# Kernel optimization log

Hardware: AMD Instinct MI355X
Metric: run time of the kernel (lower is better)

Reference implementation:

```python
import jax, jax.numpy as jnp
import numpy as np

STATE_DIM = 256
LATENT_DIM = 64
HIDDEN = 64
NUM_EMB = 2048
BATCH = 32768


def setup_inputs() -> dict:
    key = jax.random.key(0)
    ks = jax.random.split(key, 10)
    s = lambda *sh: 1.0 / np.sqrt(sh[0])
    return {
        "x": jax.random.normal(ks[0], (BATCH, STATE_DIM), dtype=jnp.float32),
        # encoder: Linear(state_dim, 64) -> ReLU -> Linear(64, latent_dim)
        "enc_w1": jax.random.uniform(ks[1], (STATE_DIM, HIDDEN), jnp.float32, -s(STATE_DIM), s(STATE_DIM)),
        "enc_b1": jax.random.uniform(ks[2], (HIDDEN,), jnp.float32, -s(STATE_DIM), s(STATE_DIM)),
        "enc_w2": jax.random.uniform(ks[3], (HIDDEN, LATENT_DIM), jnp.float32, -s(HIDDEN), s(HIDDEN)),
        "enc_b2": jax.random.uniform(ks[4], (LATENT_DIM,), jnp.float32, -s(HIDDEN), s(HIDDEN)),
        # codebook
        "emb": jax.random.normal(ks[5], (NUM_EMB, LATENT_DIM), dtype=jnp.float32),
        # decoder: Linear(latent_dim, 64) -> ReLU -> Linear(64, state_dim)
        "dec_w1": jax.random.uniform(ks[6], (LATENT_DIM, HIDDEN), jnp.float32, -s(LATENT_DIM), s(LATENT_DIM)),
        "dec_b1": jax.random.uniform(ks[7], (HIDDEN,), jnp.float32, -s(LATENT_DIM), s(LATENT_DIM)),
        "dec_w2": jax.random.uniform(ks[8], (HIDDEN, STATE_DIM), jnp.float32, -s(HIDDEN), s(HIDDEN)),
        "dec_b2": jax.random.uniform(ks[9], (STATE_DIM,), jnp.float32, -s(HIDDEN), s(HIDDEN)),
    }


def reference(x, enc_w1, enc_b1, enc_w2, enc_b2, emb, dec_w1, dec_b1, dec_w2, dec_b2):
    # encoder MLP: z_e [B, latent]
    h = jax.nn.relu(x @ enc_w1 + enc_b1)
    z_e = h @ enc_w2 + enc_b2
    # squared euclidean distances to codebook, expanded form: [B, K]
    # ||z - e||^2 = ||z||^2 - 2 z.e + ||e||^2  (same argmin as broadcast form)
    d = (jnp.sum(z_e * z_e, axis=1, keepdims=True)
         - 2.0 * (z_e @ emb.T)
         + jnp.sum(emb * emb, axis=1)[None, :])
    z_q_idx = jnp.argmin(d, axis=1)           # [B]
    z_q = emb[z_q_idx]                        # [B, latent]
    # decoder MLP
    hd = jax.nn.relu(z_q @ dec_w1 + dec_b1)
    x_recon = hd @ dec_w2 + dec_b2
    return (x_recon, z_e, z_q)
```

## Files before the change

### kernel.cpp

```cpp
#include <hip/hip_runtime.h>

#define BATCH   32768
#define SD      256
#define LD      64
#define HDIM    64
#define NEMB    2048
#define REFINE_THR_Q 5e-4f

typedef short  short8 __attribute__((ext_vector_type(8)));
typedef float  f32x4  __attribute__((ext_vector_type(4)));

__device__ __forceinline__ unsigned short f2bf(float f) {
    unsigned int u = __float_as_uint(f);
    u = (u + 0x7FFFu + ((u >> 16) & 1u)) >> 16;
    return (unsigned short)u;
}
__device__ __forceinline__ float bf2f(unsigned short h) {
    return __uint_as_float(((unsigned int)h) << 16);
}

__global__ __launch_bounds__(256) void k0_all(const float* __restrict__ emb,
                                              const float* __restrict__ dw1,
                                              const float* __restrict__ dw2,
                                              const float* __restrict__ ew1,
                                              const float* __restrict__ ew2,
                                              float* __restrict__ e2q,
                                              unsigned short* __restrict__ eh,
                                              unsigned short* __restrict__ el,
                                              unsigned short* __restrict__ w1h,
                                              unsigned short* __restrict__ w1l,
                                              unsigned short* __restrict__ w2h,
                                              unsigned short* __restrict__ w2l,
                                              unsigned short* __restrict__ w1eh,
                                              unsigned short* __restrict__ w1em,
                                              unsigned short* __restrict__ w1el,
                                              unsigned short* __restrict__ w2eh,
                                              unsigned short* __restrict__ w2em,
                                              unsigned short* __restrict__ w2el) {
    int b = blockIdx.x;
    int t = threadIdx.x;
    if (b < 8) {
        int k = b * 256 + t;
        const float* er = emb + (size_t)k * LD;
        unsigned short hrow[LD], lrow[LD];
        float s = 0.f;
#pragma unroll
        for (int q = 0; q < LD; ++q) {
            float v = er[q];
            s += v * v;
            unsigned short h = f2bf(v);
            hrow[q] = h;
            lrow[q] = f2bf(v - bf2f(h));
        }
        e2q[k] = -0.5f * s;
        short8* dh = (short8*)(eh + (size_t)k * LD);
        short8* dl = (short8*)(el + (size_t)k * LD);
#pragma unroll
        for (int q = 0; q < 8; ++q) {
            dh[q] = *(short8*)&hrow[q * 8];
            dl[q] = *(short8*)&lrow[q * 8];
        }
    } else if (b < 24) {
        int e = (b - 8) * 256 + t;
        int j = e >> 6, k = e & 63;
        float v = dw1[k * HDIM + j];
        unsigned short h = f2bf(v);
        w1h[e] = h; w1l[e] = f2bf(v - bf2f(h));
    } else if (b < 88) {
        int e = (b - 24) * 256 + t;
        int j = e >> 6, k = e & 63;
        float v = dw2[k * SD + j];
        unsigned short h = f2bf(v);
        w2h[e] = h; w2l[e] = f2bf(v - bf2f(h));
    } else if (b < 152) {
        int e = (b - 88) * 256 + t;
        int j = e >> 8, k = e & 255;
        float v = ew1[k * HDIM + j];
        unsigned short h = f2bf(v);
        float r1 = v - bf2f(h);
        unsigned short m = f2bf(r1);
        float r2 = r1 - bf2f(m);
        w1eh[e] = h; w1em[e] = m; w1el[e] = f2bf(r2);
    } else {
        int e = (b - 152) * 256 + t;
        int j = e >> 6, k = e & 63;
        float v = ew2[k * LD + j];
        unsigned short h = f2bf(v);
        float r1 = v - bf2f(h);
        unsigned short m = f2bf(r1);
        float r2 = r1 - bf2f(m);
        w2eh[e] = h; w2em[e] = m; w2el[e] = f2bf(r2);
    }
}

#define MF(Afr, Bfr, C) __builtin_amdgcn_mfma_f32_16x16x32_bf16(Afr, Bfr, C, 0, 0, 0)

__global__ __launch_bounds__(256, 2) void k_enc(const float* __restrict__ x,
                                                const unsigned short* __restrict__ w1eh,
                                                const unsigned short* __restrict__ w1em,
                                                const unsigned short* __restrict__ w1el,
                                                const float* __restrict__ b1,
                                                const unsigned short* __restrict__ w2eh,
                                                const unsigned short* __restrict__ w2em,
                                                const unsigned short* __restrict__ w2el,
                                                const float* __restrict__ b2,
                                                float* __restrict__ zOut,
                                                unsigned short* __restrict__ zh,
                                                unsigned short* __restrict__ zl) {
    __shared__ float hds[4][16 * 68];
    int tid  = threadIdx.x;
    int lane = tid & 63;
    int w    = tid >> 6;
    int lo   = lane & 15;
    int hi   = lane >> 4;
    int rb   = blockIdx.x * 64 + w * 16;
    int row  = rb + lo;

    f32x4 c1[4];
#pragma unroll
    for (int jt = 0; jt < 4; ++jt) {
        float bj = b1[jt * 16 + lo];
        f32x4 c = {bj, bj, bj, bj};
        c1[jt] = c;
    }

#pragma unroll
    for (int kt = 0; kt < 8; ++kt) {
        const float* xp = x + (size_t)row * SD + kt * 32 + hi * 8;
        float4 a4 = *(const float4*)xp;
        float4 b4 = *(const float4*)(xp + 4);
        float v[8] = {a4.x, a4.y, a4.z, a4.w, b4.x, b4.y, b4.z, b4.w};
        unsigned short sh[8], sm[8], sl[8];
#pragma unroll
        for (int q = 0; q < 8; ++q) {
            unsigned short h = f2bf(v[q]);
            float r1 = v[q] - bf2f(h);
            unsigned short m = f2bf(r1);
            float r2 = r1 - bf2f(m);
            sh[q] = h; sm[q] = m; sl[q] = f2bf(r2);
        }
        short8 ah = *(short8*)sh, am = *(short8*)sm, al = *(short8*)sl;
#pragma unroll
        for (int jt = 0; jt < 4; ++jt) {
            size_t wo = (size_t)(jt * 16 + lo) * SD + kt * 32 + hi * 8;
            short8 bh8 = *(const short8*)(w1eh + wo);
            short8 bm8 = *(const short8*)(w1em + wo);
            short8 bl8 = *(const short8*)(w1el + wo);
            f32x4 c = c1[jt];
            c = MF(al, bh8, c);
            c = MF(am, bm8, c);
            c = MF(ah, bl8, c);
            c = MF(am, bh8, c);
            c = MF(ah, bm8, c);
            c = MF(ah, bh8, c);
            c1[jt] = c;
        }
    }
#pragma unroll
    for (int jt = 0; jt < 4; ++jt)
#pragma unroll
        for (int r = 0; r < 4; ++r)
            hds[w][(hi * 4 + r) * 68 + jt * 16 + lo] = fmaxf(c1[jt][r], 0.f);
    __syncthreads();

    f32x4 c2[4];
#pragma unroll
    for (int jt = 0; jt < 4; ++jt) {
        float bj = b2[jt * 16 + lo];
        f32x4 c = {bj, bj, bj, bj};
        c2[jt] = c;
    }
#pragma unroll
    for (int kt = 0; kt < 2; ++kt) {
        float4 a4 = *(const float4*)&hds[w][lo * 68 + kt * 32 + hi * 8];
        float4 b4 = *(const float4*)&hds[w][lo * 68 + kt * 32 + hi * 8 + 4];
        float v[8] = {a4.x, a4.y, a4.z, a4.w, b4.x, b4.y, b4.z, b4.w};
        unsigned short sh[8], sm[8], sl[8];
#pragma unroll
        for (int q = 0; q < 8; ++q) {
            unsigned short h = f2bf(v[q]);
            float r1 = v[q] - bf2f(h);
            unsigned short m = f2bf(r1);
            float r2 = r1 - bf2f(m);
            sh[q] = h; sm[q] = m; sl[q] = f2bf(r2);
        }
        short8 ah = *(short8*)sh, am = *(short8*)sm, al = *(short8*)sl;
#pragma unroll
        for (int jt = 0; jt < 4; ++jt) {
            size_t wo = (size_t)(jt * 16 + lo) * LD + kt * 32 + hi * 8;
            short8 bh8 = *(const short8*)(w2eh + wo);
            short8 bm8 = *(const short8*)(w2em + wo);
            short8 bl8 = *(const short8*)(w2el + wo);
            f32x4 c = c2[jt];
            c = MF(al, bh8, c);
            c = MF(am, bm8, c);
            c = MF(ah, bl8, c);
            c = MF(am, bh8, c);
            c = MF(ah, bm8, c);
            c = MF(ah, bh8, c);
            c2[jt] = c;
        }
    }
#pragma unroll
    for (int jt = 0; jt < 4; ++jt) {
#pragma unroll
        for (int r = 0; r < 4; ++r) {
            float z = c2[jt][r];
            size_t o = (size_t)(rb + hi * 4 + r) * LD + jt * 16 + lo;
            zOut[o] = z;
            unsigned short hb = f2bf(z);
            zh[o] = hb;
            zl[o] = f2bf(z - bf2f(hb));
        }
    }
}

#define K2_LOAD(P, t) do {                                                  \
    const unsigned short* ph_ = ehp + (size_t)(t) * 16 * LD;                \
    const unsigned short* pl_ = elp + (size_t)(t) * 16 * LD;                \
    P##a0 = *(const short8*)(ph_);                                          \
    P##a1 = *(const short8*)(ph_ + 32);                                     \
    P##a2 = *(const short8*)(pl_);                                          \
    P##a3 = *(const short8*)(pl_ + 32);                                     \
    P##e2 = *(const f32x4*)(e2q + cbase + (t) * 16 + hi * 4);               \
} while (0)

#define K2_COMP(P, t) do {                                                  \
    f32x4 acc_[4];                                                          \
    _Pragma("unroll")                                                       \
    for (int g = 0; g < 4; ++g) {                                           \
        f32x4 c_;                                                           \
        c_ = __builtin_amdgcn_mfma_f32_16x16x32_bf16(P##a0, bh[g][0], P##e2, 0, 0, 0); \
        c_ = __builtin_amdgcn_mfma_f32_16x16x32_bf16(P##a1, bh[g][1], c_, 0, 0, 0);    \
        c_ = __builtin_amdgcn_mfma_f32_16x16x32_bf16(P##a2, bh[g][0], c_, 0, 0, 0);    \
        c_ = __builtin_amdgcn_mfma_f32_16x16x32_bf16(P##a3, bh[g][1], c_, 0, 0, 0);    \
        c_ = __builtin_amdgcn_mfma_f32_16x16x32_bf16(P##a0, bl[g][0], c_, 0, 0, 0);    \
        c_ = __builtin_amdgcn_mfma_f32_16x16x32_bf16(P##a1, bl[g][1], c_, 0, 0, 0);    \
        acc_[g] = c_;                                                       \
    }                                                                       \
    _Pragma("unroll")                                                       \
    for (int g = 0; g < 4; ++g) {                                           \
        float m_ = fmaxf(fmaxf(acc_[g][0], acc_[g][1]),                     \
                         fmaxf(acc_[g][2], acc_[g][3]));                    \
        bool win_ = (m_ > bb[g]);                                           \
        qv[g] = win_ ? acc_[g] : qv[g];                                     \
        tt[g] = win_ ? (t) : tt[g];                                         \
        b2v[g] = fmaxf(b2v[g], fminf(bb[g], m_));                           \
        bb[g] = fmaxf(bb[g], m_);                                           \
    }                                                                       \
} while (0)

__global__ __launch_bounds__(256, 2) void k2_mfma(const unsigned short* __restrict__ zh,
                                                  const unsigned short* __restrict__ zl,
                                                  const unsigned short* __restrict__ eh,
                                                  const unsigned short* __restrict__ el,
                                                  const float* __restrict__ e2q,
                                                  const float* __restrict__ zE,
                                                  const float* __restrict__ emb,
                                                  int* __restrict__ idx) {
    int tid  = threadIdx.x;
    int lane = tid & 63;
    int w    = tid >> 6;
    int rb   = blockIdx.x * 64;
    int lo   = lane & 15;
    int hi   = lane >> 4;

    short8 bh[4][2], bl[4][2];
#pragma unroll
    for (int g = 0; g < 4; ++g) {
        size_t zo = (size_t)(rb + g * 16 + lo) * LD + hi * 8;
        bh[g][0] = *(const short8*)(zh + zo);
        bh[g][1] = *(const short8*)(zh + zo + 32);
        bl[g][0] = *(const short8*)(zl + zo);
        bl[g][1] = *(const short8*)(zl + zo + 32);
    }

    float bb[4], b2v[4];
    f32x4 qv[4];
    int   tt[4];
#pragma unroll
    for (int g = 0; g < 4; ++g) {
        bb[g] = -3.0e38f; b2v[g] = -3.0e38f; tt[g] = 0;
        qv[g][0] = qv[g][1] = qv[g][2] = qv[g][3] = -3.0e38f;
    }

    const int cbase = w * (NEMB / 4);
    const unsigned short* ehp = eh + (size_t)(cbase + lo) * LD + hi * 8;
    const unsigned short* elp = el + (size_t)(cbase + lo) * LD + hi * 8;

    short8 Aa0, Aa1, Aa2, Aa3; f32x4 Ae2;
    short8 Ba0, Ba1, Ba2, Ba3; f32x4 Be2;
    short8 Ca0, Ca1, Ca2, Ca3; f32x4 Ce2;

    K2_LOAD(A, 0);
    K2_LOAD(B, 1);
    K2_LOAD(C, 2);

    for (int tb = 0; tb < 27; tb += 3) {
        K2_COMP(A, tb);     K2_LOAD(A, tb + 3);
        K2_COMP(B, tb + 1); K2_LOAD(B, tb + 4);
        K2_COMP(C, tb + 2); K2_LOAD(C, tb + 5);
    }
    K2_COMP(A, 27); K2_LOAD(A, 30);
    K2_COMP(B, 28); K2_LOAD(B, 31);
    K2_COMP(C, 29);
    K2_COMP(A, 30);
    K2_COMP(B, 31);

    float ss[4];
    int   ii[4];
#pragma unroll
    for (int g = 0; g < 4; ++g) {
        float s0 = qv[g][0], s1 = qv[g][1], s2 = qv[g][2], s3 = qv[g][3];
        float M01 = fmaxf(s0, s1), L01 = fminf(s0, s1);
        float M23 = fmaxf(s2, s3), L23 = fminf(s2, s3);
        int   d01 = (s1 > s0) ? 1 : 0;
        int   d23 = (s3 > s2) ? 3 : 2;
        bool  cp  = (M23 > M01);
        float within2 = fmaxf(fminf(M01, M23), cp ? L23 : L01);
        int   dd  = cp ? d23 : d01;
        ii[g] = cbase + tt[g] * 16 + hi * 4 + dd;
        ss[g] = fmaxf(b2v[g], within2);
    }

#pragma unroll
    for (int off = 16; off <= 32; off <<= 1) {
#pragma unroll
        for (int g = 0; g < 4; ++g) {
            float ob = __shfl_xor(bb[g], off);
            float os = __shfl_xor(ss[g], off);
            int   oi = __shfl_xor(ii[g], off);
            ss[g] = fmaxf(fmaxf(fminf(bb[g], ob), os), ss[g]);
            ii[g] = (ob > bb[g]) ? oi : ii[g];
            bb[g] = fmaxf(bb[g], ob);
        }
    }

    __shared__ float Lb[4][64];
    __shared__ float Ls[4][64];
    __shared__ int   Li[4][64];
    __shared__ int   flags[64];
    if (lane < 16) {
#pragma unroll
        for (int g = 0; g < 4; ++g) {
            Lb[w][g * 16 + lane] = bb[g];
            Ls[w][g * 16 + lane] = ss[g];
            Li[w][g * 16 + lane] = ii[g];
        }
    }
    __syncthreads();

    if (tid < 64) {
        float B = Lb[0][tid], S = Ls[0][tid];
        int   I = Li[0][tid];
#pragma unroll
        for (int w2 = 1; w2 < 4; ++w2) {
            float ob = Lb[w2][tid], os = Ls[w2][tid];
            int   oi = Li[w2][tid];
            S = fmaxf(fmaxf(fminf(B, ob), os), S);
            I = (ob > B) ? oi : I;
            B = fmaxf(B, ob);
        }
        idx[rb + tid] = I;
        flags[tid] = (B - S < REFINE_THR_Q) ? 1 : 0;
    }
    __syncthreads();

    __shared__ double sv[256];
    __shared__ int    sx[256];
    for (int r = 0; r < 64; ++r) {
        if (flags[r] == 0) continue;
        int rrow = rb + r;
        const float4* zr4 = (const float4*)(zE + (size_t)rrow * LD);
        float4 zv[16];
#pragma unroll
        for (int q = 0; q < 16; ++q) zv[q] = zr4[q];
        double best = 1.0e300;
        int bi = NEMB;
#pragma unroll 2
        for (int c = 0; c < 8; ++c) {
            int k = tid * 8 + c;
            const float4* er = (const float4*)(emb + (size_t)k * LD);
            double d0 = 0.0, d1 = 0.0, d2 = 0.0, d3 = 0.0;
#pragma unroll
            for (int q = 0; q < 16; ++q) {
                float4 e4 = er[q];
                double tx = (double)zv[q].x - (double)e4.x;
                double ty = (double)zv[q].y - (double)e4.y;
                double tz = (double)zv[q].z - (double)e4.z;
                double tw = (double)zv[q].w - (double)e4.w;
                d0 += tx * tx; d1 += ty * ty; d2 += tz * tz; d3 += tw * tw;
            }
            double d = (d0 + d1) + (d2 + d3);
            if (d < best) { best = d; bi = k; }
        }
        sv[tid] = best; sx[tid] = bi;
        __syncthreads();
        for (int s = 128; s > 0; s >>= 1) {
            if (tid < s) {
                if (sv[tid + s] < sv[tid] ||
                    (sv[tid + s] == sv[tid] && sx[tid + s] < sx[tid])) {
                    sv[tid] = sv[tid + s]; sx[tid] = sx[tid + s];
                }
            }
            __syncthreads();
        }
        if (tid == 0) idx[rrow] = sx[0];
        __syncthreads();
    }
}

__global__ __launch_bounds__(256, 2) void k_dec(const int* __restrict__ idx,
                                                const float* __restrict__ emb,
                                                const unsigned short* __restrict__ w1h,
                                                const unsigned short* __restrict__ w1l,
                                                const float* __restrict__ b1,
                                                const unsigned short* __restrict__ w2h,
                                                const unsigned short* __restrict__ w2l,
                                                const float* __restrict__ b2,
                                                float* __restrict__ xrec,
                                                float* __restrict__ zq) {
    __shared__ float hds[4][16 * 68];
    int tid  = threadIdx.x;
    int lane = tid & 63;
    int w    = tid >> 6;
    int lo   = lane & 15;
    int hi   = lane >> 4;
    int rb   = blockIdx.x * 64 + w * 16;
    int row  = rb + lo;
    int ix   = idx[row];

    short8 zah[2], zal[2];
    {
        const float* er  = emb + (size_t)ix * LD + hi * 8;
        float* zqr = zq + (size_t)row * LD + hi * 8;
#pragma unroll
        for (int kt = 0; kt < 2; ++kt) {
            float4 a = *(const float4*)(er + kt * 32);
            float4 b = *(const float4*)(er + kt * 32 + 4);
            *(float4*)(zqr + kt * 32) = a;
            *(float4*)(zqr + kt * 32 + 4) = b;
            float v[8] = {a.x, a.y, a.z, a.w, b.x, b.y, b.z, b.w};
            unsigned short hh[8], ll[8];
#pragma unroll
            for (int q = 0; q < 8; ++q) {
                unsigned short hb = f2bf(v[q]);
                hh[q] = hb;
                ll[q] = f2bf(v[q] - bf2f(hb));
            }
            zah[kt] = *(short8*)hh;
            zal[kt] = *(short8*)ll;
        }
    }

#pragma unroll
    for (int jt = 0; jt < 4; ++jt) {
        float bj = b1[jt * 16 + lo];
        f32x4 c = {bj, bj, bj, bj};
#pragma unroll
        for (int kt = 0; kt < 2; ++kt) {
            short8 bh8 = *(const short8*)(w1h + (jt * 16 + lo) * LD + kt * 32 + hi * 8);
            short8 bl8 = *(const short8*)(w1l + (jt * 16 + lo) * LD + kt * 32 + hi * 8);
            c = __builtin_amdgcn_mfma_f32_16x16x32_bf16(zah[kt], bh8, c, 0, 0, 0);
            c = __builtin_amdgcn_mfma_f32_16x16x32_bf16(zah[kt], bl8, c, 0, 0, 0);
            c = __builtin_amdgcn_mfma_f32_16x16x32_bf16(zal[kt], bh8, c, 0, 0, 0);
        }
#pragma unroll
        for (int r = 0; r < 4; ++r)
            hds[w][(hi * 4 + r) * 68 + jt * 16 + lo] = fmaxf(c[r], 0.f);
    }
    __syncthreads();

    short8 hah[2], hal[2];
#pragma unroll
    for (int kt = 0; kt < 2; ++kt) {
        float4 a = *(const float4*)&hds[w][lo * 68 + kt * 32 + hi * 8];
        float4 b = *(const float4*)&hds[w][lo * 68 + kt * 32 + hi * 8 + 4];
        float v[8] = {a.x, a.y, a.z, a.w, b.x, b.y, b.z, b.w};
        unsigned short hh[8], ll[8];
#pragma unroll
        for (int q = 0; q < 8; ++q) {
            unsigned short hb = f2bf(v[q]);
            hh[q] = hb;
            ll[q] = f2bf(v[q] - bf2f(hb));
        }
        hah[kt] = *(short8*)hh;
        hal[kt] = *(short8*)ll;
    }

    for (int jt = 0; jt < 16; ++jt) {
        float bj = b2[jt * 16 + lo];
        f32x4 c = {bj, bj, bj, bj};
#pragma unroll
        for (int kt = 0; kt < 2; ++kt) {
            short8 bh8 = *(const short8*)(w2h + (jt * 16 + lo) * LD + kt * 32 + hi * 8);
            short8 bl8 = *(const short8*)(w2l + (jt * 16 + lo) * LD + kt * 32 + hi * 8);
            c = __builtin_amdgcn_mfma_f32_16x16x32_bf16(hah[kt], bh8, c, 0, 0, 0);
            c = __builtin_amdgcn_mfma_f32_16x16x32_bf16(hah[kt], bl8, c, 0, 0, 0);
            c = __builtin_amdgcn_mfma_f32_16x16x32_bf16(hal[kt], bh8, c, 0, 0, 0);
        }
#pragma unroll
        for (int r = 0; r < 4; ++r)
            xrec[(size_t)(rb + hi * 4 + r) * SD + jt * 16 + lo] = c[r];
    }
}

extern "C" void kernel_launch(void* const* d_in, const int* in_sizes, int n_in,
                              void* d_out, int out_size, void* d_ws, size_t ws_size,
                              hipStream_t stream) {
    const float* x   = (const float*)d_in[0];
    const float* ew1 = (const float*)d_in[1];
    const float* eb1 = (const float*)d_in[2];
    const float* ew2 = (const float*)d_in[3];
    const float* eb2 = (const float*)d_in[4];
    const float* emb = (const float*)d_in[5];
    const float* dw1 = (const float*)d_in[6];
    const float* db1 = (const float*)d_in[7];
    const float* dw2 = (const float*)d_in[8];
    const float* db2 = (const float*)d_in[9];

    float* out  = (float*)d_out;
    float* xrec = out;
    float* zE   = out + (size_t)BATCH * SD;
    float* zQ   = zE + (size_t)BATCH * LD;

    char* xb = (char*)xrec;
    unsigned short* zh   = (unsigned short*)xb;
    unsigned short* zl   = (unsigned short*)(xb + (4u << 20));
    unsigned short* eh   = (unsigned short*)(xb + (8u << 20));
    unsigned short* el   = (unsigned short*)(xb + (8u << 20) + (NEMB * LD * 2));
    float*          e2q  = (float*)(xb + (9u << 20));
    unsigned short* w1eh = (unsigned short*)(xb + (10u << 20));
    unsigned short* w1em = w1eh + 16384;
    unsigned short* w1el = w1em + 16384;
    unsigned short* w2eh = w1el + 16384;
    unsigned short* w2em = w2eh + 4096;
    unsigned short* w2el = w2em + 4096;

    char* ws = (char*)d_ws;
    int*  idxA  = (int*)(ws + 16384);
    unsigned short* w1h = (unsigned short*)(ws + 278528);
    unsigned short* w1l = (unsigned short*)(ws + 286720);
    unsigned short* w2h = (unsigned short*)(ws + 294912);
    unsigned short* w2l = (unsigned short*)(ws + 327680);

    hipLaunchKernelGGL(k0_all,  dim3(168),        dim3(256), 0, stream,
                       emb, dw1, dw2, ew1, ew2, e2q, eh, el,
                       w1h, w1l, w2h, w2l, w1eh, w1em, w1el, w2eh, w2em, w2el);
    hipLaunchKernelGGL(k_enc,   dim3(BATCH / 64), dim3(256), 0, stream,
                       x, w1eh, w1em, w1el, eb1, w2eh, w2em, w2el, eb2, zE, zh, zl);
    hipLaunchKernelGGL(k2_mfma, dim3(BATCH / 64), dim3(256), 0, stream,
                       zh, zl, eh, el, e2q, zE, emb, idxA);
    hipLaunchKernelGGL(k_dec,   dim3(BATCH / 64), dim3(256), 0, stream,
                       idxA, emb, w1h, w1l, db1, w2h, w2l, db2, xrec, zQ);
}
```

Before: 128.7 us.

## Move near-tie argmin refinement into separate kernel with atomic work list

Blocks in the MFMA distance kernel no longer refine ambiguous rows themselves. Instead they append each flagged row index to a global list through an atomic counter. A new 128-block kernel then walks that compacted list and runs the fp64 exact-distance refinement. This is meant to remove load imbalance and tail latency from blocks that hit many near-tie rows. The cost is an extra kernel launch, an atomic per flagged row, and possibly uneven work if few rows are flagged.

```diff
diff --git a/kernel.cpp b/kernel.cpp
--- a/kernel.cpp
+++ b/kernel.cpp
@@ -36,11 +36,13 @@
                                               unsigned short* __restrict__ w1el,
                                               unsigned short* __restrict__ w2eh,
                                               unsigned short* __restrict__ w2em,
-                                              unsigned short* __restrict__ w2el) {
+                                              unsigned short* __restrict__ w2el,
+                                              int* __restrict__ count) {
     int b = blockIdx.x;
     int t = threadIdx.x;
     if (b < 8) {
         int k = b * 256 + t;
+        if (k == 0) *count = 0;
         const float* er = emb + (size_t)k * LD;
         unsigned short hrow[LD], lrow[LD];
         float s = 0.f;
@@ -255,9 +257,9 @@
                                                   const unsigned short* __restrict__ eh,
                                                   const unsigned short* __restrict__ el,
                                                   const float* __restrict__ e2q,
-                                                  const float* __restrict__ zE,
-                                                  const float* __restrict__ emb,
-                                                  int* __restrict__ idx) {
+                                                  int* __restrict__ idx,
+                                                  int* __restrict__ list,
+                                                  int* __restrict__ count) {
     int tid  = threadIdx.x;
     int lane = tid & 63;
     int w    = tid >> 6;
@@ -339,7 +341,6 @@
     __shared__ float Lb[4][64];
     __shared__ float Ls[4][64];
     __shared__ int   Li[4][64];
-    __shared__ int   flags[64];
     if (lane < 16) {
 #pragma unroll
         for (int g = 0; g < 4; ++g) {
@@ -362,19 +363,29 @@
             B = fmaxf(B, ob);
         }
         idx[rb + tid] = I;
-        flags[tid] = (B - S < REFINE_THR_Q) ? 1 : 0;
-    }
-    __syncthreads();
-
+        if (B - S < REFINE_THR_Q) {
+            int p = atomicAdd(count, 1);
+            list[p] = rb + tid;
+        }
+    }
+}
+
+__global__ __launch_bounds__(256) void k3_refine(const float* __restrict__ z,
+                                                 const float* __restrict__ emb,
+                                                 const int* __restrict__ count,
+                                                 const int* __restrict__ list,
+                                                 int* __restrict__ idx) {
     __shared__ double sv[256];
     __shared__ int    sx[256];
-    for (int r = 0; r < 64; ++r) {
-        if (flags[r] == 0) continue;
-        int rrow = rb + r;
-        const float4* zr4 = (const float4*)(zE + (size_t)rrow * LD);
+    int tid = threadIdx.x;
+    int n = *count;
+    for (int g = blockIdx.x; g < n; g += gridDim.x) {
+        int row = list[g];
+        const float4* zr4 = (const float4*)(z + (size_t)row * LD);
         float4 zv[16];
 #pragma unroll
         for (int q = 0; q < 16; ++q) zv[q] = zr4[q];
+
         double best = 1.0e300;
         int bi = NEMB;
 #pragma unroll 2
@@ -405,7 +416,7 @@
             }
             __syncthreads();
         }
-        if (tid == 0) idx[rrow] = sx[0];
+        if (tid == 0) idx[row] = sx[0];
         __syncthreads();
     }
 }
@@ -538,19 +549,23 @@
     unsigned short* w2el = w2em + 4096;
 
     char* ws = (char*)d_ws;
+    int*  count = (int*)ws;
     int*  idxA  = (int*)(ws + 16384);
+    int*  list  = (int*)(ws + 147456);
     unsigned short* w1h = (unsigned short*)(ws + 278528);
     unsigned short* w1l = (unsigned short*)(ws + 286720);
     unsigned short* w2h = (unsigned short*)(ws + 294912);
     unsigned short* w2l = (unsigned short*)(ws + 327680);
 
-    hipLaunchKernelGGL(k0_all,  dim3(168),        dim3(256), 0, stream,
+    hipLaunchKernelGGL(k0_all,    dim3(168),        dim3(256), 0, stream,
                        emb, dw1, dw2, ew1, ew2, e2q, eh, el,
-                       w1h, w1l, w2h, w2l, w1eh, w1em, w1el, w2eh, w2em, w2el);
-    hipLaunchKernelGGL(k_enc,   dim3(BATCH / 64), dim3(256), 0, stream,
+                       w1h, w1l, w2h, w2l, w1eh, w1em, w1el, w2eh, w2em, w2el, count);
+    hipLaunchKernelGGL(k_enc,     dim3(BATCH / 64), dim3(256), 0, stream,
                        x, w1eh, w1em, w1el, eb1, w2eh, w2em, w2el, eb2, zE, zh, zl);
-    hipLaunchKernelGGL(k2_mfma, dim3(BATCH / 64), dim3(256), 0, stream,
-                       zh, zl, eh, el, e2q, zE, emb, idxA);
-    hipLaunchKernelGGL(k_dec,   dim3(BATCH / 64), dim3(256), 0, stream,
+    hipLaunchKernelGGL(k2_mfma,   dim3(BATCH / 64), dim3(256), 0, stream,
+                       zh, zl, eh, el, e2q, idxA, list, count);
+    hipLaunchKernelGGL(k3_refine, dim3(128),        dim3(256), 0, stream,
+                       zE, emb, count, list, idxA);
+    hipLaunchKernelGGL(k_dec,     dim3(BATCH / 64), dim3(256), 0, stream,
                        idxA, emb, w1h, w1l, db1, w2h, w2l, db2, xrec, zQ);
 }
```

Measured after the change: 128.0 us. No clear change (-0.6%).
